# Kernel optimization log

Hardware: AMD Instinct MI355X
Metric: run time of the kernel (lower is better)

The kernel has to match this reference:

```python
import jax, jax.numpy as jnp
import numpy as np

NUM_HEADS = 4


def setup_inputs() -> dict:
    key = jax.random.key(0)
    ks = jax.random.split(key, 8)
    B, N, C = 4096, 49, 128  # num_windows*batch, Wh*Ww, embed_dims
    nW = 64                  # windows per image
    x = jax.random.normal(ks[0], (B, N, C), dtype=jnp.float32)
    mask = jax.random.normal(ks[1], (nW, N, N), dtype=jnp.float32)
    w_qkv = jax.random.normal(ks[2], (3 * C, C), dtype=jnp.float32) * (C ** -0.5)
    b_qkv = jax.random.normal(ks[3], (3 * C,), dtype=jnp.float32) * 0.02
    w_proj = jax.random.normal(ks[4], (C, C), dtype=jnp.float32) * (C ** -0.5)
    b_proj = jax.random.normal(ks[5], (C,), dtype=jnp.float32) * 0.02
    bias_table = jax.random.normal(ks[6], (169, NUM_HEADS), dtype=jnp.float32) * 0.02
    rel_index = jax.random.randint(ks[7], (N, N), 0, 169, dtype=jnp.int64)
    return {"x": x, "mask": mask, "w_qkv": w_qkv, "b_qkv": b_qkv,
            "w_proj": w_proj, "b_proj": b_proj,
            "bias_table": bias_table, "rel_index": rel_index}


def reference(x, mask, w_qkv, b_qkv, w_proj, b_proj, bias_table, rel_index):
    B, N, C = x.shape
    H = NUM_HEADS
    D = C // H
    scale = D ** -0.5
    # qkv projection: (B,N,3C) -> (3,B,H,N,D)
    qkv = (x @ w_qkv.T + b_qkv).reshape(B, N, 3, H, D).transpose(2, 0, 3, 1, 4)
    q, k, v = qkv[0], qkv[1], qkv[2]
    attn = jnp.einsum('bhnd,bhmd->bhnm', q * scale, k)  # (B,H,N,N)
    # gathered relative-position bias: (N,N,H) -> (H,N,N)
    rpb = bias_table[rel_index.reshape(-1)].reshape(N, N, H).transpose(2, 0, 1)
    attn = attn + rpb[None]
    # shift-window mask: (nW,N,N) broadcast over batch-per-window and heads
    nW = mask.shape[0]
    attn = attn.reshape(B // nW, nW, H, N, N) + mask[None, :, None]
    attn = attn.reshape(B, H, N, N)
    attn = jax.nn.softmax(attn, axis=-1)  # attn_drop is identity in eval
    out = jnp.einsum('bhnm,bhmd->bhnd', attn, v)
    out = out.transpose(0, 2, 1, 3).reshape(B, N, C)
    out = out @ w_proj.T + b_proj  # proj_drop is identity in eval
    return out
```

## Files before the change

kernel.cpp:

```cpp
#include <hip/hip_runtime.h>
#include <hip/hip_bf16.h>

typedef __attribute__((ext_vector_type(4))) float f32x4;
typedef __attribute__((ext_vector_type(8))) __bf16 bf16x8;
typedef __attribute__((ext_vector_type(4))) __bf16 bf16x4;

#define MFMA_BF16(a, b, c) __builtin_amdgcn_mfma_f32_16x16x32_bf16((a), (b), (c), 0, 0, 0)

static __device__ __forceinline__ __bf16 f2b(float f) {
    return __builtin_bit_cast(__bf16, __float2bfloat16(f));
}
static __device__ __forceinline__ unsigned short f2u(float f) {
    return __builtin_bit_cast(unsigned short, __float2bfloat16(f));
}

__global__ void prep_kernel(const float* __restrict__ w_qkv, const float* __restrict__ b_qkv,
                            const float* __restrict__ w_proj, const float* __restrict__ mask,
                            const float* __restrict__ table, const int* __restrict__ rel,
                            unsigned short* __restrict__ wqkv_b, unsigned short* __restrict__ wproj_b,
                            float* __restrict__ bqkv_s, float* __restrict__ cmb) {
    const float s = 0.17677669529663687f;
    int i = blockIdx.x * 256 + threadIdx.x;
    if (i < 49152) {
        int n = i >> 7;
        wqkv_b[i] = f2u(w_qkv[i] * (n < 128 ? s : 1.0f));
    } else if (i < 49536) {
        int j = i - 49152;
        bqkv_s[j] = b_qkv[j] * (j < 128 ? s : 1.0f);
    } else if (i < 65920) {
        int e = i - 49536;
        wproj_b[e] = f2u(w_proj[e]);
    } else if (i < 680576) {
        int c = i - 65920;
        int wi = c / 9604;
        int r2 = c - wi * 9604;
        int h = r2 / 2401;
        int mn = r2 - h * 2401;
        cmb[c] = mask[wi * 2401 + mn] + table[rel[mn] * 4 + h];
    }
}

__global__ __launch_bounds__(256, 2) void fused_kernel(
    const float* __restrict__ x, const unsigned short* __restrict__ wqkv_b,
    const float* __restrict__ bqkv_s, const unsigned short* __restrict__ wproj_b,
    const float* __restrict__ b_proj, const float* __restrict__ cmb,
    float* __restrict__ out) {
    __shared__ __align__(16) char smem[65536];

    const int b = blockIdx.x;
    const int tid = threadIdx.x;
    const int lane = tid & 63;
    const int h = tid >> 6;
    const int wi = b & 63;

    char* xos = smem;
    char* qkp = smem + 16384 + h * 8192;
    char* vts = smem + 49152 + h * 4096;

    {
        const float* xb = x + (size_t)b * 49 * 128;
        for (int i = tid; i < 2048; i += 256) {
            int row = i >> 5, c4 = (i & 31) * 4;
            float4 v = {0.f, 0.f, 0.f, 0.f};
            if (row < 49) v = *(const float4*)(xb + row * 128 + c4);
            bf16x4 bv = {f2b(v.x), f2b(v.y), f2b(v.z), f2b(v.w)};
            *(bf16x4*)(xos + row * 256 + ((c4 * 2) ^ ((row & 7) << 4))) = bv;
        }
    }
    __syncthreads();

    const int rb = (lane >> 4) * 4;
    const int cI = lane & 15;

    {
        bf16x8 af[4][4];
#pragma unroll
        for (int mt = 0; mt < 4; ++mt)
#pragma unroll
            for (int kc = 0; kc < 4; ++kc) {
                int row = mt * 16 + cI;
                af[mt][kc] = *(const bf16x8*)(xos + row * 256 +
                                              ((kc * 64 + (lane >> 4) * 16) ^ ((row & 7) << 4)));
            }
#pragma unroll
        for (int ct = 0; ct < 6; ++ct) {
            int n0 = (ct < 2) ? h * 32 + ct * 16
                              : (ct < 4) ? 128 + h * 32 + (ct - 2) * 16
                                         : 256 + h * 32 + (ct - 4) * 16;
            bf16x8 bfr[4];
#pragma unroll
            for (int kc = 0; kc < 4; ++kc)
                bfr[kc] = *(const bf16x8*)(wqkv_b + (size_t)(n0 + cI) * 128 + kc * 32 +
                                           (lane >> 4) * 8);
            f32x4 acc[4] = {};
#pragma unroll
            for (int mt = 0; mt < 4; ++mt)
#pragma unroll
                for (int kc = 0; kc < 4; ++kc)
                    acc[mt] = MFMA_BF16(af[mt][kc], bfr[kc], acc[mt]);
            float bias = bqkv_s[n0 + cI];
            if (ct < 4) {
                char* base = qkp + ((ct < 2) ? 0 : 4096);
                int d = (ct & 1) * 16 + cI;
#pragma unroll
                for (int mt = 0; mt < 4; ++mt)
#pragma unroll
                    for (int r = 0; r < 4; ++r) {
                        int t = mt * 16 + rb + r;
                        *(__bf16*)(base + t * 64 + ((d * 2) ^ ((t & 3) << 4))) =
                            f2b(acc[mt][r] + bias);
                    }
            } else {
                int d = (ct & 1) * 16 + cI;
#pragma unroll
                for (int mt = 0; mt < 4; ++mt) {
                    int t0 = mt * 16 + rb;
                    bf16x4 pv = {f2b(acc[mt][0] + bias), f2b(acc[mt][1] + bias),
                                 f2b(acc[mt][2] + bias), f2b(acc[mt][3] + bias)};
                    *(bf16x4*)(vts + d * 128 + ((t0 * 2) ^ ((d & 7) << 4))) = pv;
                }
            }
        }
    }
    __syncthreads();

    f32x4 S[4][4] = {};
    {
        bf16x8 qf[4], kf[4];
#pragma unroll
        for (int mt = 0; mt < 4; ++mt) {
            int row = mt * 16 + cI;
            qf[mt] = *(const bf16x8*)(qkp + row * 64 + (((lane >> 4) * 16) ^ ((row & 3) << 4)));
        }
#pragma unroll
        for (int nt = 0; nt < 4; ++nt) {
            int row = nt * 16 + cI;
            kf[nt] = *(const bf16x8*)(qkp + 4096 + row * 64 +
                                      (((lane >> 4) * 16) ^ ((row & 3) << 4)));
        }
#pragma unroll
        for (int mt = 0; mt < 4; ++mt)
#pragma unroll
            for (int nt = 0; nt < 4; ++nt)
                S[mt][nt] = MFMA_BF16(qf[mt], kf[nt], S[mt][nt]);
    }
    {
        const float* cw = cmb + ((size_t)wi * 4 + h) * 2401;
#pragma unroll
        for (int mt = 0; mt < 4; ++mt)
#pragma unroll
            for (int nt = 0; nt < 4; ++nt)
#pragma unroll
                for (int r = 0; r < 4; ++r) {
                    int m = mt * 16 + rb + r, n = nt * 16 + cI;
                    if (m < 49 && n < 49)
                        S[mt][nt][r] += cw[m * 49 + n];
                    else
                        S[mt][nt][r] = -1e30f;
                }
    }
    float sm[4][4];
#pragma unroll
    for (int mt = 0; mt < 4; ++mt)
#pragma unroll
        for (int r = 0; r < 4; ++r) {
            float v = fmaxf(fmaxf(S[mt][0][r], S[mt][1][r]), fmaxf(S[mt][2][r], S[mt][3][r]));
            v = fmaxf(v, __shfl_xor(v, 1));
            v = fmaxf(v, __shfl_xor(v, 2));
            v = fmaxf(v, __shfl_xor(v, 4));
            v = fmaxf(v, __shfl_xor(v, 8));
            sm[mt][r] = v;
        }
#pragma unroll
    for (int mt = 0; mt < 4; ++mt)
#pragma unroll
        for (int nt = 0; nt < 4; ++nt)
#pragma unroll
            for (int r = 0; r < 4; ++r)
                S[mt][nt][r] = __expf(S[mt][nt][r] - sm[mt][r]);
#pragma unroll
    for (int mt = 0; mt < 4; ++mt)
#pragma unroll
        for (int r = 0; r < 4; ++r) {
            float v = S[mt][0][r] + S[mt][1][r] + S[mt][2][r] + S[mt][3][r];
            v += __shfl_xor(v, 1);
            v += __shfl_xor(v, 2);
            v += __shfl_xor(v, 4);
            v += __shfl_xor(v, 8);
            sm[mt][r] = 1.0f / v;
        }
#pragma unroll
    for (int mt = 0; mt < 4; ++mt)
#pragma unroll
        for (int nt = 0; nt < 4; ++nt)
#pragma unroll
            for (int r = 0; r < 4; ++r) {
                int m = mt * 16 + rb + r, n = nt * 16 + cI;
                *(__bf16*)(qkp + m * 128 + ((n * 2) ^ ((m & 7) << 4))) = f2b(S[mt][nt][r]);
            }

    f32x4 Oa[4][2] = {};
#pragma unroll
    for (int kt = 0; kt < 2; ++kt) {
        const int kb = kt * 64 + (lane >> 4) * 16;
        bf16x8 pf[4], vf[2];
#pragma unroll
        for (int mt = 0; mt < 4; ++mt) {
            int row = mt * 16 + cI;
            pf[mt] = *(const bf16x8*)(qkp + row * 128 + (kb ^ ((row & 7) << 4)));
        }
#pragma unroll
        for (int nd = 0; nd < 2; ++nd) {
            int row = nd * 16 + cI;
            vf[nd] = *(const bf16x8*)(vts + row * 128 + (kb ^ ((row & 7) << 4)));
        }
#pragma unroll
        for (int mt = 0; mt < 4; ++mt)
#pragma unroll
            for (int nd = 0; nd < 2; ++nd)
                Oa[mt][nd] = MFMA_BF16(pf[mt], vf[nd], Oa[mt][nd]);
    }

#pragma unroll
    for (int mt = 0; mt < 4; ++mt)
#pragma unroll
        for (int nd = 0; nd < 2; ++nd)
#pragma unroll
            for (int r = 0; r < 4; ++r) {
                int t = mt * 16 + rb + r;
                int c = h * 32 + nd * 16 + cI;
                *(__bf16*)(xos + t * 256 + ((c * 2) ^ ((t & 7) << 4))) =
                    f2b(Oa[mt][nd][r] * sm[mt][r]);
            }
    __syncthreads();

    {
        bf16x8 af[4][4];
#pragma unroll
        for (int mt = 0; mt < 4; ++mt)
#pragma unroll
            for (int kc = 0; kc < 4; ++kc) {
                int row = mt * 16 + cI;
                af[mt][kc] = *(const bf16x8*)(xos + row * 256 +
                                              ((kc * 64 + (lane >> 4) * 16) ^ ((row & 7) << 4)));
            }
#pragma unroll
        for (int ct = 0; ct < 2; ++ct) {
            int n0 = h * 32 + ct * 16;
            bf16x8 bfr[4];
#pragma unroll
            for (int kc = 0; kc < 4; ++kc)
                bfr[kc] = *(const bf16x8*)(wproj_b + (size_t)(n0 + cI) * 128 + kc * 32 +
                                           (lane >> 4) * 8);
            f32x4 acc[4] = {};
#pragma unroll
            for (int mt = 0; mt < 4; ++mt)
#pragma unroll
                for (int kc = 0; kc < 4; ++kc)
                    acc[mt] = MFMA_BF16(af[mt][kc], bfr[kc], acc[mt]);
            float bias = b_proj[n0 + cI];
#pragma unroll
            for (int mt = 0; mt < 4; ++mt)
#pragma unroll
                for (int r = 0; r < 4; ++r) {
                    int t = mt * 16 + rb + r;
                    if (t < 49)
                        out[((size_t)b * 49 + t) * 128 + n0 + cI] = acc[mt][r] + bias;
                }
        }
    }
}

extern "C" void kernel_launch(void* const* d_in, const int* in_sizes, int n_in,
                              void* d_out, int out_size, void* d_ws, size_t ws_size,
                              hipStream_t stream) {
    (void)in_sizes; (void)n_in; (void)out_size; (void)ws_size;
    const float* x      = (const float*)d_in[0];
    const float* mask   = (const float*)d_in[1];
    const float* w_qkv  = (const float*)d_in[2];
    const float* b_qkv  = (const float*)d_in[3];
    const float* w_proj = (const float*)d_in[4];
    const float* b_proj = (const float*)d_in[5];
    const float* btab   = (const float*)d_in[6];
    const int*   rel    = (const int*)d_in[7];
    float* out = (float*)d_out;

    char* ws = (char*)d_ws;
    unsigned short* wqkv_b  = (unsigned short*)(ws);
    unsigned short* wproj_b = (unsigned short*)(ws + 98304);
    float*          bqkv_s  = (float*)(ws + 131072);
    float*          cmb     = (float*)(ws + 132608);

    prep_kernel<<<2659, 256, 0, stream>>>(w_qkv, b_qkv, w_proj, mask, btab, rel,
                                          wqkv_b, wproj_b, bqkv_s, cmb);
    fused_kernel<<<4096, 256, 0, stream>>>(x, wqkv_b, bqkv_s, wproj_b, b_proj, cmb, out);
}
```

Baseline: 309.0 us.

## Split each head across two waves with 512-thread blocks

Result: faster. 294.5 us (-4.7%).

```diff
diff --git a/kernel.cpp b/kernel.cpp
--- a/kernel.cpp
+++ b/kernel.cpp
@@ -40,7 +40,11 @@
     }
 }
 
-__global__ __launch_bounds__(256, 2) void fused_kernel(
+static __device__ __forceinline__ int qk_addr(int t, int off) {
+    return (t * 64 + off) ^ ((t & 7) << 4);
+}
+
+__global__ __launch_bounds__(512, 4) void fused_kernel(
     const float* __restrict__ x, const unsigned short* __restrict__ wqkv_b,
     const float* __restrict__ bqkv_s, const unsigned short* __restrict__ wproj_b,
     const float* __restrict__ b_proj, const float* __restrict__ cmb,
@@ -50,16 +54,21 @@
     const int b = blockIdx.x;
     const int tid = threadIdx.x;
     const int lane = tid & 63;
-    const int h = tid >> 6;
+    const int w = tid >> 6;
+    const int h = w >> 1;
+    const int q = w & 1;
     const int wi = b & 63;
 
     char* xos = smem;
-    char* qkp = smem + 16384 + h * 8192;
-    char* vts = smem + 49152 + h * 4096;
+    char* qkp = smem + 16384 + h * 12288;
+    char* vts = qkp + 8192;
+
+    const int rb = (lane >> 4) * 4;
+    const int cI = lane & 15;
 
     {
         const float* xb = x + (size_t)b * 49 * 128;
-        for (int i = tid; i < 2048; i += 256) {
+        for (int i = tid; i < 2048; i += 512) {
             int row = i >> 5, c4 = (i & 31) * 4;
             float4 v = {0.f, 0.f, 0.f, 0.f};
             if (row < 49) v = *(const float4*)(xb + row * 128 + c4);
@@ -69,9 +78,6 @@
     }
     __syncthreads();
 
-    const int rb = (lane >> 4) * 4;
-    const int cI = lane & 15;
-
     {
         bf16x8 af[4][4];
 #pragma unroll
@@ -83,10 +89,8 @@
                                               ((kc * 64 + (lane >> 4) * 16) ^ ((row & 7) << 4)));
             }
 #pragma unroll
-        for (int ct = 0; ct < 6; ++ct) {
-            int n0 = (ct < 2) ? h * 32 + ct * 16
-                              : (ct < 4) ? 128 + h * 32 + (ct - 2) * 16
-                                         : 256 + h * 32 + (ct - 4) * 16;
+        for (int t3 = 0; t3 < 3; ++t3) {
+            int n0 = t3 * 128 + w * 16;
             bf16x8 bfr[4];
 #pragma unroll
             for (int kc = 0; kc < 4; ++kc)
@@ -99,115 +103,113 @@
                 for (int kc = 0; kc < 4; ++kc)
                     acc[mt] = MFMA_BF16(af[mt][kc], bfr[kc], acc[mt]);
             float bias = bqkv_s[n0 + cI];
-            if (ct < 4) {
-                char* base = qkp + ((ct < 2) ? 0 : 4096);
-                int d = (ct & 1) * 16 + cI;
+            int dl = q * 16 + cI;
+            if (t3 < 2) {
+                char* base = qkp + t3 * 4096;
 #pragma unroll
                 for (int mt = 0; mt < 4; ++mt)
 #pragma unroll
                     for (int r = 0; r < 4; ++r) {
                         int t = mt * 16 + rb + r;
-                        *(__bf16*)(base + t * 64 + ((d * 2) ^ ((t & 3) << 4))) =
-                            f2b(acc[mt][r] + bias);
+                        *(__bf16*)(base + qk_addr(t, dl * 2)) = f2b(acc[mt][r] + bias);
                     }
             } else {
-                int d = (ct & 1) * 16 + cI;
 #pragma unroll
                 for (int mt = 0; mt < 4; ++mt) {
                     int t0 = mt * 16 + rb;
                     bf16x4 pv = {f2b(acc[mt][0] + bias), f2b(acc[mt][1] + bias),
                                  f2b(acc[mt][2] + bias), f2b(acc[mt][3] + bias)};
-                    *(bf16x4*)(vts + d * 128 + ((t0 * 2) ^ ((d & 7) << 4))) = pv;
+                    *(bf16x4*)(vts + dl * 128 + ((t0 * 2) ^ ((dl & 7) << 4))) = pv;
                 }
             }
         }
     }
     __syncthreads();
 
-    f32x4 S[4][4] = {};
-    {
-        bf16x8 qf[4], kf[4];
-#pragma unroll
-        for (int mt = 0; mt < 4; ++mt) {
-            int row = mt * 16 + cI;
-            qf[mt] = *(const bf16x8*)(qkp + row * 64 + (((lane >> 4) * 16) ^ ((row & 3) << 4)));
+    f32x4 S[2][4] = {};
+    {
+        bf16x8 qf[2], kf[4];
+#pragma unroll
+        for (int j = 0; j < 2; ++j) {
+            int row = (2 * q + j) * 16 + cI;
+            qf[j] = *(const bf16x8*)(qkp + qk_addr(row, (lane >> 4) * 16));
         }
 #pragma unroll
         for (int nt = 0; nt < 4; ++nt) {
             int row = nt * 16 + cI;
-            kf[nt] = *(const bf16x8*)(qkp + 4096 + row * 64 +
-                                      (((lane >> 4) * 16) ^ ((row & 3) << 4)));
-        }
-#pragma unroll
-        for (int mt = 0; mt < 4; ++mt)
+            kf[nt] = *(const bf16x8*)(qkp + 4096 + qk_addr(row, (lane >> 4) * 16));
+        }
+#pragma unroll
+        for (int j = 0; j < 2; ++j)
 #pragma unroll
             for (int nt = 0; nt < 4; ++nt)
-                S[mt][nt] = MFMA_BF16(qf[mt], kf[nt], S[mt][nt]);
-    }
+                S[j][nt] = MFMA_BF16(qf[j], kf[nt], S[j][nt]);
+    }
+    __syncthreads();
     {
         const float* cw = cmb + ((size_t)wi * 4 + h) * 2401;
 #pragma unroll
-        for (int mt = 0; mt < 4; ++mt)
+        for (int j = 0; j < 2; ++j)
 #pragma unroll
             for (int nt = 0; nt < 4; ++nt)
 #pragma unroll
                 for (int r = 0; r < 4; ++r) {
-                    int m = mt * 16 + rb + r, n = nt * 16 + cI;
+                    int m = (2 * q + j) * 16 + rb + r, n = nt * 16 + cI;
                     if (m < 49 && n < 49)
-                        S[mt][nt][r] += cw[m * 49 + n];
+                        S[j][nt][r] += cw[m * 49 + n];
                     else
-                        S[mt][nt][r] = -1e30f;
+                        S[j][nt][r] = -1e30f;
                 }
     }
-    float sm[4][4];
-#pragma unroll
-    for (int mt = 0; mt < 4; ++mt)
+    float sm[2][4];
+#pragma unroll
+    for (int j = 0; j < 2; ++j)
 #pragma unroll
         for (int r = 0; r < 4; ++r) {
-            float v = fmaxf(fmaxf(S[mt][0][r], S[mt][1][r]), fmaxf(S[mt][2][r], S[mt][3][r]));
+            float v = fmaxf(fmaxf(S[j][0][r], S[j][1][r]), fmaxf(S[j][2][r], S[j][3][r]));
             v = fmaxf(v, __shfl_xor(v, 1));
             v = fmaxf(v, __shfl_xor(v, 2));
             v = fmaxf(v, __shfl_xor(v, 4));
             v = fmaxf(v, __shfl_xor(v, 8));
-            sm[mt][r] = v;
-        }
-#pragma unroll
-    for (int mt = 0; mt < 4; ++mt)
+            sm[j][r] = v;
+        }
+#pragma unroll
+    for (int j = 0; j < 2; ++j)
 #pragma unroll
         for (int nt = 0; nt < 4; ++nt)
 #pragma unroll
             for (int r = 0; r < 4; ++r)
-                S[mt][nt][r] = __expf(S[mt][nt][r] - sm[mt][r]);
-#pragma unroll
-    for (int mt = 0; mt < 4; ++mt)
+                S[j][nt][r] = __expf(S[j][nt][r] - sm[j][r]);
+#pragma unroll
+    for (int j = 0; j < 2; ++j)
 #pragma unroll
         for (int r = 0; r < 4; ++r) {
-            float v = S[mt][0][r] + S[mt][1][r] + S[mt][2][r] + S[mt][3][r];
+            float v = S[j][0][r] + S[j][1][r] + S[j][2][r] + S[j][3][r];
             v += __shfl_xor(v, 1);
             v += __shfl_xor(v, 2);
             v += __shfl_xor(v, 4);
             v += __shfl_xor(v, 8);
-            sm[mt][r] = 1.0f / v;
-        }
-#pragma unroll
-    for (int mt = 0; mt < 4; ++mt)
+            sm[j][r] = 1.0f / v;
+        }
+#pragma unroll
+    for (int j = 0; j < 2; ++j)
 #pragma unroll
         for (int nt = 0; nt < 4; ++nt)
 #pragma unroll
             for (int r = 0; r < 4; ++r) {
-                int m = mt * 16 + rb + r, n = nt * 16 + cI;
-                *(__bf16*)(qkp + m * 128 + ((n * 2) ^ ((m & 7) << 4))) = f2b(S[mt][nt][r]);
-            }
-
-    f32x4 Oa[4][2] = {};
+                int m = (2 * q + j) * 16 + rb + r, n = nt * 16 + cI;
+                *(__bf16*)(qkp + m * 128 + ((n * 2) ^ ((m & 7) << 4))) = f2b(S[j][nt][r]);
+            }
+
+    f32x4 Oa[2][2] = {};
 #pragma unroll
     for (int kt = 0; kt < 2; ++kt) {
         const int kb = kt * 64 + (lane >> 4) * 16;
-        bf16x8 pf[4], vf[2];
-#pragma unroll
-        for (int mt = 0; mt < 4; ++mt) {
-            int row = mt * 16 + cI;
-            pf[mt] = *(const bf16x8*)(qkp + row * 128 + (kb ^ ((row & 7) << 4)));
+        bf16x8 pf[2], vf[2];
+#pragma unroll
+        for (int j = 0; j < 2; ++j) {
+            int row = (2 * q + j) * 16 + cI;
+            pf[j] = *(const bf16x8*)(qkp + row * 128 + (kb ^ ((row & 7) << 4)));
         }
 #pragma unroll
         for (int nd = 0; nd < 2; ++nd) {
@@ -215,22 +217,22 @@
             vf[nd] = *(const bf16x8*)(vts + row * 128 + (kb ^ ((row & 7) << 4)));
         }
 #pragma unroll
-        for (int mt = 0; mt < 4; ++mt)
+        for (int j = 0; j < 2; ++j)
 #pragma unroll
             for (int nd = 0; nd < 2; ++nd)
-                Oa[mt][nd] = MFMA_BF16(pf[mt], vf[nd], Oa[mt][nd]);
-    }
-
-#pragma unroll
-    for (int mt = 0; mt < 4; ++mt)
+                Oa[j][nd] = MFMA_BF16(pf[j], vf[nd], Oa[j][nd]);
+    }
+
+#pragma unroll
+    for (int j = 0; j < 2; ++j)
 #pragma unroll
         for (int nd = 0; nd < 2; ++nd)
 #pragma unroll
             for (int r = 0; r < 4; ++r) {
-                int t = mt * 16 + rb + r;
+                int t = (2 * q + j) * 16 + rb + r;
                 int c = h * 32 + nd * 16 + cI;
                 *(__bf16*)(xos + t * 256 + ((c * 2) ^ ((t & 7) << 4))) =
-                    f2b(Oa[mt][nd][r] * sm[mt][r]);
+                    f2b(Oa[j][nd][r] * sm[j][r]);
             }
     __syncthreads();
 
@@ -244,30 +246,27 @@
                 af[mt][kc] = *(const bf16x8*)(xos + row * 256 +
                                               ((kc * 64 + (lane >> 4) * 16) ^ ((row & 7) << 4)));
             }
-#pragma unroll
-        for (int ct = 0; ct < 2; ++ct) {
-            int n0 = h * 32 + ct * 16;
-            bf16x8 bfr[4];
+        int n0 = w * 16;
+        bf16x8 bfr[4];
+#pragma unroll
+        for (int kc = 0; kc < 4; ++kc)
+            bfr[kc] = *(const bf16x8*)(wproj_b + (size_t)(n0 + cI) * 128 + kc * 32 +
+                                       (lane >> 4) * 8);
+        f32x4 acc[4] = {};
+#pragma unroll
+        for (int mt = 0; mt < 4; ++mt)
 #pragma unroll
             for (int kc = 0; kc < 4; ++kc)
-                bfr[kc] = *(const bf16x8*)(wproj_b + (size_t)(n0 + cI) * 128 + kc * 32 +
-                                           (lane >> 4) * 8);
-            f32x4 acc[4] = {};
-#pragma unroll
-            for (int mt = 0; mt < 4; ++mt)
-#pragma unroll
-                for (int kc = 0; kc < 4; ++kc)
-                    acc[mt] = MFMA_BF16(af[mt][kc], bfr[kc], acc[mt]);
-            float bias = b_proj[n0 + cI];
-#pragma unroll
-            for (int mt = 0; mt < 4; ++mt)
-#pragma unroll
-                for (int r = 0; r < 4; ++r) {
-                    int t = mt * 16 + rb + r;
-                    if (t < 49)
-                        out[((size_t)b * 49 + t) * 128 + n0 + cI] = acc[mt][r] + bias;
-                }
-        }
+                acc[mt] = MFMA_BF16(af[mt][kc], bfr[kc], acc[mt]);
+        float bias = b_proj[n0 + cI];
+#pragma unroll
+        for (int mt = 0; mt < 4; ++mt)
+#pragma unroll
+            for (int r = 0; r < 4; ++r) {
+                int t = mt * 16 + rb + r;
+                if (t < 49)
+                    out[((size_t)b * 49 + t) * 128 + n0 + cI] = acc[mt][r] + bias;
+            }
     }
 }
 
@@ -293,5 +292,5 @@
 
     prep_kernel<<<2659, 256, 0, stream>>>(w_qkv, b_qkv, w_proj, mask, btab, rel,
                                           wqkv_b, wproj_b, bqkv_s, cmb);
-    fused_kernel<<<4096, 256, 0, stream>>>(x, wqkv_b, bqkv_s, wproj_b, b_proj, cmb, out);
-}
+    fused_kernel<<<4096, 512, 0, stream>>>(x, wqkv_b, bqkv_s, wproj_b, b_proj, cmb, out);
+}
```
